# Kernel tuning notes

Hardware: AMD Instinct MI355X
Metric: run time of the kernel (lower is better)

The kernel has to match this reference:

```python
import jax, jax.numpy as jnp
import numpy as np
from jax import lax

DIM = 1024
DIM_INNER = 2048  # int(dim * expansion_factor)


def log_g(x):
    # log-space g(x): where(x>=0, log(relu(x)+0.5), -softplus(-x))
    return jnp.where(x >= 0, jnp.log(jax.nn.relu(x) + 0.5), -jax.nn.softplus(-x))


def heinsen_associative_scan_log(log_coeffs, log_values):
    # parallel log-space linear recurrence over the sequence axis (axis=1)
    a_star = jnp.cumsum(log_coeffs, axis=1)
    log_h0_plus_b_star = lax.cumlogsumexp(log_values - a_star, axis=1)
    return a_star + log_h0_plus_b_star


def setup_inputs() -> dict:
    key = jax.random.key(0)
    k_x, k_w1, k_w2 = jax.random.split(key, 3)
    x = jax.random.normal(k_x, (4, 4096, DIM), dtype=jnp.float32)
    # Linear(dim, 2*dim_inner, bias=False): store as [in, out] for x @ W
    W_hg = jax.random.normal(k_w1, (DIM, 2 * DIM_INNER), dtype=jnp.float32) * (1.0 / np.sqrt(DIM))
    W_out = jax.random.normal(k_w2, (DIM_INNER, DIM), dtype=jnp.float32) * (1.0 / np.sqrt(DIM_INNER))
    return {"x": x, "W_hg": W_hg, "W_out": W_out}


def reference(x, W_hg, W_out):
    # x: [b, s, dim]
    hg = jnp.einsum('bsd,de->bse', x, W_hg)  # [b, s, 2*dim_inner]
    hidden, gate = jnp.split(hg, 2, axis=-1)
    log_coeffs = -jax.nn.softplus(gate)        # log(1 - z)
    log_z = -jax.nn.softplus(-gate)            # log z
    log_values = log_z + log_g(hidden)
    log_h = heinsen_associative_scan_log(log_coeffs, log_values)  # [b, s, dim_inner]
    out = jnp.exp(log_h)
    return jnp.einsum('bse,ed->bsd', out, W_out)
```

## Files before the change

### kernel.cpp

```cpp
#include <hip/hip_runtime.h>
#include <cmath>

#define DIM 1024
#define DIM_INNER 2048
#define BATCH 4
#define SEQ 4096
#define MTOT (BATCH * SEQ)
#define CHUNK 32
#define NCHUNK (SEQ / CHUNK)

typedef __bf16 bf16x8 __attribute__((ext_vector_type(8)));
typedef short short8_t __attribute__((ext_vector_type(8)));
typedef float floatx4 __attribute__((ext_vector_type(4)));
typedef unsigned short u16x4 __attribute__((ext_vector_type(4)));
typedef unsigned int uint4_t __attribute__((ext_vector_type(4)));
typedef float float4_t __attribute__((ext_vector_type(4)));
typedef unsigned short ushort_t;

template <int N> struct IC { static constexpr int v = N; };
template <bool B> struct BC { static constexpr bool v = B; };

#define LGKM_SB(n) do { asm volatile("s_waitcnt lgkmcnt(" #n ")" ::: "memory"); \
                        __builtin_amdgcn_sched_barrier(0); } while (0)
#define SCHED0() __builtin_amdgcn_sched_barrier(0)
#define SBAR() __builtin_amdgcn_s_barrier()
#define PRIO1() __builtin_amdgcn_s_setprio(1)
#define PRIO0() __builtin_amdgcn_s_setprio(0)

__device__ __forceinline__ unsigned short f2bf(float f) {
  unsigned int u = __builtin_bit_cast(unsigned int, f);
  u += 0x7fffu + ((u >> 16) & 1u);
  return (unsigned short)(u >> 16);
}
__device__ __forceinline__ float bflo2f(unsigned int u) {
  return __builtin_bit_cast(float, u << 16);
}
__device__ __forceinline__ float bfhi2f(unsigned int u) {
  return __builtin_bit_cast(float, u & 0xffff0000u);
}

__device__ __forceinline__ void lclv_fast(float h, float g, float& lc, float& lv) {
  float eg = __expf(-fabsf(g));
  float sp = fmaxf(g, 0.f) + __logf(1.f + eg);
  lc = -sp;
  float eh = __expf(h);
  float t  = (h >= 0.f) ? (h + 0.5f) : (1.f + eh);
  float lt = __logf(t);
  float lg = (h >= 0.f) ? lt : (h - lt);
  lv = g + lc + lg;
}
__device__ __forceinline__ float logaddexp_f(float a, float b) {
  float m = fmaxf(a, b);
  return m + __logf(1.f + __expf(-fabsf(a - b)));
}

__device__ __forceinline__ void async_copy16(const ushort_t* g, ushort_t* l) {
  __builtin_amdgcn_global_load_lds(
      (const __attribute__((address_space(1))) void*)g,
      (__attribute__((address_space(3))) void*)l, 16, 0, 0);
}

__global__ __launch_bounds__(256) void convert_f32_bf16(
    const float* __restrict__ src, ushort_t* __restrict__ dst) {
  int i = blockIdx.x * 256 + threadIdx.x;
  float4 v = ((const float4*)src)[i];
  u16x4 o = {f2bf(v.x), f2bf(v.y), f2bf(v.z), f2bf(v.w)};
  ((u16x4*)dst)[i] = o;
}

__global__ __launch_bounds__(256) void transpose_f32_bf16(
    const float* __restrict__ src, ushort_t* __restrict__ dst, int K, int N) {
  __shared__ float tile[32][33];
  int tx = threadIdx.x & 31, ty = threadIdx.x >> 5;
  int n0 = blockIdx.x * 32, k0 = blockIdx.y * 32;
#pragma unroll
  for (int i = 0; i < 4; i++) {
    int k = ty + i * 8;
    tile[k][tx] = src[(size_t)(k0 + k) * N + n0 + tx];
  }
  __syncthreads();
#pragma unroll
  for (int i = 0; i < 4; i++) {
    int r = ty + i * 8;
    dst[(size_t)(n0 + r) * K + k0 + tx] = f2bf(tile[tx][r]);
  }
}

#define G1_NT (DIM / 64)
#define G2_NT (DIM_INNER / 64)

__global__ __launch_bounds__(512, 2) void gemm1_fused(
    const ushort_t* __restrict__ Xbf, const ushort_t* __restrict__ Wt,
    unsigned int* __restrict__ LCLV,
    float* __restrict__ Asum, float* __restrict__ Lend, int nbch) {
  __shared__ __align__(16) ushort_t lds[81920];

  const int tid = threadIdx.x;
  const int wv = tid >> 6;
  const int lane = tid & 63;
  const int wr = wv >> 2;
  const int wc = wv & 3;
  const int l15 = lane & 15;
  const int quad = lane >> 4;
  const int n0 = blockIdx.x * 128;
  const int m0 = blockIdx.y * 256;

  int aSrc[2][2], bSrc[2][2];
  int dstE[2];
#pragma unroll
  for (int L = 0; L < 2; L++) {
    int e = L * 512 + tid;
    int row = e >> 3, slot = e & 7;
    int sw = (slot ^ (row & 7)) << 3;
    dstE[L] = e * 8;
#pragma unroll
    for (int half = 0; half < 2; half++) {
      aSrc[half][L] = (m0 + half * 128 + row) * DIM + sw;
      int br = half * 128 + row;
      int grow = n0 + ((br >> 6) << 5) + (br & 31) + ((br & 32) ? DIM_INNER : 0);
      bSrc[half][L] = grow * DIM + sw;
    }
  }

  auto stageA = [&](int kt, int half, int buf) {
#pragma unroll
    for (int L = 0; L < 2; L++)
      async_copy16(Xbf + aSrc[half][L] + kt * 64,
                   lds + buf * 16384 + half * 8192 + dstE[L]);
  };
  auto stageB = [&](int kt, int half, int buf) {
#pragma unroll
    for (int L = 0; L < 2; L++)
      async_copy16(Wt + bSrc[half][L] + kt * 64,
                   lds + 49152 + buf * 16384 + half * 8192 + dstE[L]);
  };

  const int swz0 = ((quad ^ (l15 & 7)) << 3);
  const int swz1 = (((4 | quad) ^ (l15 & 7)) << 3);
  const int aB0 = wr * 8192 + l15 * 64 + swz0;
  const int aB1 = wr * 8192 + l15 * 64 + swz1;
  const int bB0 = wc * 4096 + l15 * 64 + swz0;
  const int bB1 = wc * 4096 + l15 * 64 + swz1;

  auto readA = [&](int buf, int mf, int ks) -> bf16x8 {
    const ushort_t* p = lds + buf * 16384 + (ks ? aB1 : aB0) + mf * 1024;
    return __builtin_bit_cast(bf16x8, *(const short8_t*)p);
  };
  auto readB = [&](int buf, int nf, int ks) -> bf16x8 {
    const ushort_t* p = lds + 49152 + buf * 16384 + (ks ? bB1 : bB0) + nf * 1024;
    return __builtin_bit_cast(bf16x8, *(const short8_t*)p);
  };

  floatx4 acc[8][4];
#pragma unroll
  for (int i = 0; i < 8; i++)
#pragma unroll
    for (int j = 0; j < 4; j++) acc[i][j] = (floatx4){0.f, 0.f, 0.f, 0.f};

  bf16x8 aF[4][2], b0F[2][2], b1F[2][2];

  auto mma4 = [&](auto MA, auto MC, auto J, bf16x8 (&bX)[2][2]) {
#pragma unroll
    for (int jj = 0; jj < 2; jj++)
#pragma unroll
      for (int ks = 0; ks < 2; ks++)
        acc[MC.v][J.v + jj] = __builtin_amdgcn_mfma_f32_16x16x32_bf16(
            aF[MA.v][ks], bX[jj][ks], acc[MC.v][J.v + jj], 0, 0, 0);
  };
  auto mmaRow = [&](auto J, bf16x8 (&bvec)[2]) {
#pragma unroll
    for (int m = 0; m < 4; m++)
#pragma unroll
      for (int ks = 0; ks < 2; ks++)
        acc[m][J.v] = __builtin_amdgcn_mfma_f32_16x16x32_bf16(
            aF[m][ks], bvec[ks], acc[m][J.v], 0, 0, 0);
  };

  int bufA = 0, bufB = 0, bufAn = 2, bufBn = 1;

  auto tileBody = [&](int kb, int ka, auto STB, auto STA, auto VMALL) {
    aF[0][0] = readA(bufA, 0, 0); aF[0][1] = readA(bufA, 0, 1);
    b0F[0][0] = readB(bufB, 0, 0); b0F[0][1] = readB(bufB, 0, 1);
    b0F[1][0] = readB(bufB, 1, 0); b0F[1][1] = readB(bufB, 1, 1);
    SCHED0();
    aF[1][0] = readA(bufA, 1, 0); aF[1][1] = readA(bufA, 1, 1);
    SCHED0();
    aF[2][0] = readA(bufA, 2, 0); aF[2][1] = readA(bufA, 2, 1);
    SCHED0();
    aF[3][0] = readA(bufA, 3, 0); aF[3][1] = readA(bufA, 3, 1);
    SCHED0();
    if constexpr (STB.v) stageB(kb, 0, bufBn);
    SBAR();
    PRIO1();
    LGKM_SB(6); mma4(IC<0>{}, IC<0>{}, IC<0>{}, b0F);
    LGKM_SB(4); mma4(IC<1>{}, IC<1>{}, IC<0>{}, b0F);
    LGKM_SB(2); mma4(IC<2>{}, IC<2>{}, IC<0>{}, b0F);
    LGKM_SB(0); mma4(IC<3>{}, IC<3>{}, IC<0>{}, b0F);
    PRIO0();
    SBAR();

    b1F[0][0] = readB(bufB, 2, 0); b1F[0][1] = readB(bufB, 2, 1);
    SCHED0();
    b1F[1][0] = readB(bufB, 3, 0); b1F[1][1] = readB(bufB, 3, 1);
    SCHED0();
    if constexpr (STB.v) stageB(kb, 1, bufBn);
    SBAR();
    PRIO1();
    LGKM_SB(2); mmaRow(IC<2>{}, b1F[0]);
    LGKM_SB(0); mmaRow(IC<3>{}, b1F[1]);
    PRIO0();
    SBAR();

    aF[0][0] = readA(bufA, 4, 0); aF[0][1] = readA(bufA, 4, 1);
    SCHED0();
    aF[1][0] = readA(bufA, 5, 0); aF[1][1] = readA(bufA, 5, 1);
    SCHED0();
    aF[2][0] = readA(bufA, 6, 0); aF[2][1] = readA(bufA, 6, 1);
    SCHED0();
    aF[3][0] = readA(bufA, 7, 0); aF[3][1] = readA(bufA, 7, 1);
    SCHED0();
    if constexpr (STA.v) stageA(ka, 0, bufAn);
    SBAR();
    PRIO1();
    LGKM_SB(6); mma4(IC<0>{}, IC<4>{}, IC<2>{}, b1F);
    LGKM_SB(4); mma4(IC<1>{}, IC<5>{}, IC<2>{}, b1F);
    LGKM_SB(2); mma4(IC<2>{}, IC<6>{}, IC<2>{}, b1F);
    LGKM_SB(0); mma4(IC<3>{}, IC<7>{}, IC<2>{}, b1F);
    PRIO0();
    SBAR();

    if constexpr (STA.v) stageA(ka, 1, bufAn);
    SCHED0();
    if constexpr (STA.v) {
      asm volatile("s_waitcnt vmcnt(4)" ::: "memory");
    } else if constexpr (VMALL.v) {
      asm volatile("s_waitcnt vmcnt(0)" ::: "memory");
    }
    SBAR();
    PRIO1();
    mma4(IC<0>{}, IC<4>{}, IC<0>{}, b0F);
    mma4(IC<1>{}, IC<5>{}, IC<0>{}, b0F);
    mma4(IC<2>{}, IC<6>{}, IC<0>{}, b0F);
    mma4(IC<3>{}, IC<7>{}, IC<0>{}, b0F);
    PRIO0();
    SBAR();
  };

  stageB(0, 0, 0); stageB(0, 1, 0);
  stageA(0, 0, 0); stageA(0, 1, 0);
  stageA(1, 0, 1); stageA(1, 1, 1);
  asm volatile("s_waitcnt vmcnt(4)" ::: "memory");
  SBAR();

  for (int u = 0; u < G1_NT - 2; u++) {
    tileBody(u + 1, u + 2, BC<true>{}, BC<true>{}, BC<false>{});
    bufA = (bufA == 2) ? 0 : bufA + 1;
    bufAn = (bufAn == 2) ? 0 : bufAn + 1;
    bufB ^= 1; bufBn ^= 1;
  }
  tileBody(G1_NT - 1, 0, BC<true>{}, BC<false>{}, BC<true>{});
  bufA = (bufA == 2) ? 0 : bufA + 1;
  bufB ^= 1;
  tileBody(0, 0, BC<false>{}, BC<false>{}, BC<false>{});

#pragma unroll
  for (int c2 = 0; c2 < 4; c2++) {
    float hA[2][2], hL[2][2];
#pragma unroll
    for (int mh = 0; mh < 2; mh++) {
      int mf = c2 * 2 + mh;
#pragma unroll
      for (int j = 0; j < 2; j++) {
        int col = n0 + wc * 32 + j * 16 + l15;
        float sA = 0.f, sL = -INFINITY;
#pragma unroll
        for (int r = 0; r < 4; r++) {
          int row = m0 + wr * 128 + mf * 16 + quad * 4 + r;
          float lc, lv;
          lclv_fast(acc[mf][j][r], acc[mf][j + 2][r], lc, lv);
          unsigned int pk = ((unsigned int)f2bf(lv) << 16) | (unsigned int)f2bf(lc);
          LCLV[(size_t)row * DIM_INNER + col] = pk;
          sL = logaddexp_f(sL + lc, lv);
          sA += lc;
        }
        float A = sA, L = sL;
#pragma unroll
        for (int st = 16; st <= 32; st <<= 1) {
          float Ao = __shfl_xor(A, st, 64);
          float Lo = __shfl_xor(L, st, 64);
          bool upper = (lane & st) != 0;
          L = upper ? logaddexp_f(Lo + A, L) : logaddexp_f(L + Ao, Lo);
          A = A + Ao;
        }
        hA[mh][j] = A;
        hL[mh][j] = L;
      }
    }
#pragma unroll
    for (int j = 0; j < 2; j++) {
      float A = hA[0][j] + hA[1][j];
      float L = logaddexp_f(hL[0][j] + hA[1][j], hL[1][j]);
      if (quad == 0) {
        int cg = (m0 + wr * 128 + c2 * 32) >> 5;
        int bz = cg >> 7;
        int cs = cg & (NCHUNK - 1);
        int col = n0 + wc * 32 + j * 16 + l15;
        size_t sidx = (size_t)cs * nbch + (size_t)bz * DIM_INNER + col;
        Asum[sidx] = A;
        Lend[sidx] = L;
      }
    }
  }
}

#define A0OFF 0
#define A1OFF 16384
#define B0OFF 32768
#define B1OFF 49152

__global__ __launch_bounds__(512, 2) void gemm2(
    const ushort_t* __restrict__ Hbf, const ushort_t* __restrict__ Wot,
    float* __restrict__ OUT) {
  __shared__ __align__(16) ushort_t lds[65536];

  const int tid = threadIdx.x;
  const int lane = tid & 63;
  const int wv = tid >> 6;
  const int wr = wv >> 2;
  const int wc = wv & 3;
  const int l15 = lane & 15;
  const int quad = lane >> 4;
  const int n0 = blockIdx.x * 256;
  const int m0 = blockIdx.y * 256;

  int aSrc[2][2], bSrc[2][2];
  int dstE[2];
#pragma unroll
  for (int L = 0; L < 2; L++) {
    int e = L * 512 + tid;
    int row = e >> 3, slot = e & 7;
    int sw = (slot ^ (row & 7)) << 3;
    dstE[L] = e * 8;
#pragma unroll
    for (int half = 0; half < 2; half++) {
      aSrc[half][L] = (m0 + half * 128 + row) * DIM_INNER + sw;
      bSrc[half][L] = (n0 + half * 128 + row) * DIM_INNER + sw;
    }
  }

  auto stA = [&](int kt, int half, auto AO) {
#pragma unroll
    for (int L = 0; L < 2; L++)
      async_copy16(Hbf + aSrc[half][L] + kt * 64,
                   lds + AO.v + half * 8192 + dstE[L]);
  };
  auto stB = [&](int kt, int half, auto BO) {
#pragma unroll
    for (int L = 0; L < 2; L++)
      async_copy16(Wot + bSrc[half][L] + kt * 64,
                   lds + BO.v + half * 8192 + dstE[L]);
  };

  const int swz0 = ((quad ^ (l15 & 7)) << 3);
  const int swz1 = (((4 | quad) ^ (l15 & 7)) << 3);
  const int aB0 = wr * 8192 + l15 * 64 + swz0;
  const int aB1 = wr * 8192 + l15 * 64 + swz1;
  const int bB0 = wc * 4096 + l15 * 64 + swz0;
  const int bB1 = wc * 4096 + l15 * 64 + swz1;

  floatx4 acc[8][4];
#pragma unroll
  for (int i = 0; i < 8; i++)
#pragma unroll
    for (int j = 0; j < 4; j++) acc[i][j] = (floatx4){0.f, 0.f, 0.f, 0.f};

  bf16x8 aF[4][2], b0F[2][2], b1F[2][2];

  auto rdA4 = [&](auto AO, int mb) {
#pragma unroll
    for (int m = 0; m < 4; m++) {
      aF[m][0] = __builtin_bit_cast(bf16x8,
          *(const short8_t*)(lds + AO.v + aB0 + (mb + m) * 1024));
      aF[m][1] = __builtin_bit_cast(bf16x8,
          *(const short8_t*)(lds + AO.v + aB1 + (mb + m) * 1024));
    }
  };
  auto rdB2 = [&](auto BO, int nb, bf16x8 (&bX)[2][2]) {
#pragma unroll
    for (int n = 0; n < 2; n++) {
      bX[n][0] = __builtin_bit_cast(bf16x8,
          *(const short8_t*)(lds + BO.v + bB0 + (nb + n) * 1024));
      bX[n][1] = __builtin_bit_cast(bf16x8,
          *(const short8_t*)(lds + BO.v + bB1 + (nb + n) * 1024));
    }
  };
  auto mmaQ = [&](auto MB, auto JB, bf16x8 (&bX)[2][2]) {
#pragma unroll
    for (int m = 0; m < 4; m++)
#pragma unroll
      for (int jj = 0; jj < 2; jj++)
#pragma unroll
        for (int ks = 0; ks < 2; ks++)
          acc[MB.v + m][JB.v + jj] = __builtin_amdgcn_mfma_f32_16x16x32_bf16(
              aF[m][ks], bX[jj][ks], acc[MB.v + m][JB.v + jj], 0, 0, 0);
  };

  auto pairBody = [&](int k2, auto STG) {
    rdA4(IC<A0OFF>{}, 0); rdB2(IC<B0OFF>{}, 0, b0F);
    SCHED0();
    SBAR(); LGKM_SB(0);
    PRIO1(); mmaQ(IC<0>{}, IC<0>{}, b0F); PRIO0();
    SBAR();
    rdB2(IC<B0OFF>{}, 2, b1F);
    SCHED0();
    SBAR(); LGKM_SB(0);
    PRIO1(); mmaQ(IC<0>{}, IC<2>{}, b1F); PRIO0();
    SBAR();
    rdA4(IC<A0OFF>{}, 4);
    SCHED0();
    if constexpr (STG.v) stB(k2, 0, IC<B0OFF>{});
    SBAR(); LGKM_SB(0);
    PRIO1(); mmaQ(IC<4>{}, IC<2>{}, b1F); PRIO0();
    SBAR();
    if constexpr (STG.v) {
      stB(k2, 1, IC<B0OFF>{});
      asm volatile("s_waitcnt vmcnt(4)" ::: "memory");
    } else {
      asm volatile("s_waitcnt vmcnt(0)" ::: "memory");
    }
    SBAR();
    PRIO1(); mmaQ(IC<4>{}, IC<0>{}, b0F); PRIO0();
    SBAR();
    rdA4(IC<A1OFF>{}, 0); rdB2(IC<B1OFF>{}, 0, b0F);
    SCHED0();
    if constexpr (STG.v) stA(k2, 0, IC<A0OFF>{});
    SBAR(); LGKM_SB(0);
    PRIO1(); mmaQ(IC<0>{}, IC<0>{}, b0F); PRIO0();
    SBAR();
    rdB2(IC<B1OFF>{}, 2, b1F);
    SCHED0();
    if constexpr (STG.v) stA(k2, 1, IC<A0OFF>{});
    SBAR(); LGKM_SB(0);
    PRIO1(); mmaQ(IC<0>{}, IC<2>{}, b1F); PRIO0();
    SBAR();
    rdA4(IC<A1OFF>{}, 4);
    SCHED0();
    if constexpr (STG.v) stB(k2 + 1, 0, IC<B1OFF>{});
    SBAR(); LGKM_SB(0);
    PRIO1(); mmaQ(IC<4>{}, IC<2>{}, b1F); PRIO0();
    SBAR();
    if constexpr (STG.v) {
      stB(k2 + 1, 1, IC<B1OFF>{});
      stA(k2 + 1, 0, IC<A1OFF>{});
      stA(k2 + 1, 1, IC<A1OFF>{});
      asm volatile("s_waitcnt vmcnt(8)" ::: "memory");
    }
    SBAR();
    PRIO1(); mmaQ(IC<4>{}, IC<0>{}, b0F); PRIO0();
    SBAR();
  };

  stA(0, 0, IC<A0OFF>{}); stA(0, 1, IC<A0OFF>{});
  stB(0, 0, IC<B0OFF>{}); stB(0, 1, IC<B0OFF>{});
  stA(1, 0, IC<A1OFF>{}); stA(1, 1, IC<A1OFF>{});
  stB(1, 0, IC<B1OFF>{}); stB(1, 1, IC<B1OFF>{});
  asm volatile("s_waitcnt vmcnt(8)" ::: "memory");
  SBAR();

  for (int it = 0; it < G2_NT / 2 - 1; ++it)
    pairBody(2 * it + 2, BC<true>{});
  pairBody(0, BC<false>{});

#pragma unroll
  for (int mf = 0; mf < 8; mf++)
#pragma unroll
    for (int j = 0; j < 4; j++) {
      int col = n0 + wc * 64 + (j >> 1) * 32 + (j & 1) * 16 + l15;
#pragma unroll
      for (int r = 0; r < 4; r++) {
        int row = m0 + wr * 128 + mf * 16 + quad * 4 + r;
        OUT[(size_t)row * DIM + col] = acc[mf][j][r];
      }
    }
}


__global__ __launch_bounds__(256) void scan_phase2(
    float* Asum, const float* __restrict__ Lend, int nbch) {
  int ch = blockIdx.x * 256 + threadIdx.x;
  float p = -INFINITY;
  for (int c = 0; c < NCHUNK; c++) {
    float a = Asum[(size_t)c * nbch + ch];
    float le = Lend[(size_t)c * nbch + ch];
    Asum[(size_t)c * nbch + ch] = p;
    p = logaddexp_f(a + p, le);
  }
}

__global__ __launch_bounds__(256) void scan_phase3(
    const unsigned int* __restrict__ LCLV, const float* __restrict__ P,
    ushort_t* __restrict__ H, int nbch) {
  const int EQ = DIM_INNER / 4;
  int tid = blockIdx.x * 256 + threadIdx.x;
  int ep = tid % EQ;
  int tmp = tid / EQ;
  int c = tmp % NCHUNK;
  int bz = tmp / NCHUNK;
  size_t base4 = ((size_t)bz * SEQ + (size_t)c * CHUNK) * EQ + ep;
  const uint4_t* L4 = (const uint4_t*)LCLV;
  u16x4* H4 = (u16x4*)H;

  size_t pidx = ((size_t)c * nbch + (size_t)bz * DIM_INNER) / 4 + ep;
  float4_t logh = ((const float4_t*)P)[pidx];
#pragma unroll 4
  for (int t = 0; t < CHUNK; t++) {
    uint4_t u = L4[base4 + (size_t)t * EQ];
    u16x4 hv;
#pragma unroll
    for (int k = 0; k < 4; k++) {
      float lc = bflo2f(u[k]), lv = bfhi2f(u[k]);
      logh[k] = logaddexp_f(lc + logh[k], lv);
      hv[k] = f2bf(__expf(logh[k]));
    }
    H4[base4 + (size_t)t * EQ] = hv;
  }
}

extern "C" void kernel_launch(void* const* d_in, const int* in_sizes, int n_in,
                              void* d_out, int out_size, void* d_ws, size_t ws_size,
                              hipStream_t stream) {
  const float* X = (const float*)d_in[0];
  const float* Whg = (const float*)d_in[1];
  const float* Wout = (const float*)d_in[2];
  float* out = (float*)d_out;

  ushort_t* Xbf = (ushort_t*)d_ws;
  ushort_t* Whg_t = Xbf + (size_t)MTOT * DIM;
  ushort_t* Wout_t = Whg_t + (size_t)(2 * DIM_INNER) * DIM;
  char* pp = (char*)(Wout_t + (size_t)DIM * DIM_INNER);

  const size_t fixed_bytes = (size_t)MTOT * DIM * 2 +
                             (size_t)2 * DIM_INNER * DIM * 2 +
                             (size_t)DIM * DIM_INNER * 2;
  const size_t per_batch = (size_t)SEQ * DIM_INNER * 4 +
                           (size_t)SEQ * DIM_INNER * 2 +
                           2 * (size_t)DIM_INNER * NCHUNK * 4;
  int nb = 4;
  while (nb > 1 && fixed_bytes + (size_t)nb * per_batch > ws_size) nb >>= 1;
  const int npass = BATCH / nb;

  convert_f32_bf16<<<(MTOT * DIM / 4) / 256, 256, 0, stream>>>(X, Xbf);
  transpose_f32_bf16<<<dim3(2 * DIM_INNER / 32, DIM / 32), 256, 0, stream>>>(
      Whg, Whg_t, DIM, 2 * DIM_INNER);
  transpose_f32_bf16<<<dim3(DIM / 32, DIM_INNER / 32), 256, 0, stream>>>(
      Wout, Wout_t, DIM_INNER, DIM);

  for (int pass = 0; pass < npass; pass++) {
    const int b0 = pass * nb;
    const int nrows = nb * SEQ;
    const int nbch = nb * DIM_INNER;

    unsigned int* LCLV = (unsigned int*)pp;
    ushort_t* Hbf = (ushort_t*)(LCLV + (size_t)nb * SEQ * DIM_INNER);
    float* Asum = (float*)(Hbf + (size_t)nb * SEQ * DIM_INNER);
    float* Lend = Asum + (size_t)nb * DIM_INNER * NCHUNK;

    gemm1_fused<<<dim3(DIM_INNER / 128, nrows / 256), 512, 0, stream>>>(
        Xbf + (size_t)b0 * SEQ * DIM, Whg_t, LCLV, Asum, Lend, nbch);
    scan_phase2<<<nbch / 256, 256, 0, stream>>>(Asum, Lend, nbch);
    scan_phase3<<<(nbch / 4 * NCHUNK) / 256, 256, 0, stream>>>(LCLV, Asum, Hbf, nbch);
    gemm2<<<dim3(DIM / 256, nrows / 256), 512, 0, stream>>>(
        Hbf, Wout_t, out + (size_t)b0 * SEQ * DIM);
  }
}
```

Before: 447.2 us.

## Unfuse chunk summary scan from GEMM1 epilogue into separate phase1 kernel

Moves the per-chunk scan summary (sum of log coefficients and log-sum-exp end value) out of the GEMM1 epilogue into a new scan_phase1 kernel that re-reads the packed LCLV buffer. This makes the GEMM epilogue lighter, dropping its cross-lane shuffles and transcendental work, which may also ease register pressure. In exchange it costs an extra launch and a full extra read of LCLV. Phase2 is also changed to batch eight chunk loads before its serial recurrence, to hide memory latency.

```diff
diff --git a/kernel.cpp b/kernel.cpp
--- a/kernel.cpp
+++ b/kernel.cpp
@@ -91,8 +91,7 @@
 
 __global__ __launch_bounds__(512, 2) void gemm1_fused(
     const ushort_t* __restrict__ Xbf, const ushort_t* __restrict__ Wt,
-    unsigned int* __restrict__ LCLV,
-    float* __restrict__ Asum, float* __restrict__ Lend, int nbch) {
+    unsigned int* __restrict__ LCLV) {
   __shared__ __align__(16) ushort_t lds[81920];
 
   const int tid = threadIdx.x;
@@ -264,53 +263,19 @@
   tileBody(0, 0, BC<false>{}, BC<false>{}, BC<false>{});
 
 #pragma unroll
-  for (int c2 = 0; c2 < 4; c2++) {
-    float hA[2][2], hL[2][2];
-#pragma unroll
-    for (int mh = 0; mh < 2; mh++) {
-      int mf = c2 * 2 + mh;
-#pragma unroll
-      for (int j = 0; j < 2; j++) {
-        int col = n0 + wc * 32 + j * 16 + l15;
-        float sA = 0.f, sL = -INFINITY;
-#pragma unroll
-        for (int r = 0; r < 4; r++) {
-          int row = m0 + wr * 128 + mf * 16 + quad * 4 + r;
-          float lc, lv;
-          lclv_fast(acc[mf][j][r], acc[mf][j + 2][r], lc, lv);
-          unsigned int pk = ((unsigned int)f2bf(lv) << 16) | (unsigned int)f2bf(lc);
-          LCLV[(size_t)row * DIM_INNER + col] = pk;
-          sL = logaddexp_f(sL + lc, lv);
-          sA += lc;
-        }
-        float A = sA, L = sL;
-#pragma unroll
-        for (int st = 16; st <= 32; st <<= 1) {
-          float Ao = __shfl_xor(A, st, 64);
-          float Lo = __shfl_xor(L, st, 64);
-          bool upper = (lane & st) != 0;
-          L = upper ? logaddexp_f(Lo + A, L) : logaddexp_f(L + Ao, Lo);
-          A = A + Ao;
-        }
-        hA[mh][j] = A;
-        hL[mh][j] = L;
+  for (int mf = 0; mf < 8; mf++)
+#pragma unroll
+    for (int j = 0; j < 2; j++) {
+      int col = n0 + wc * 32 + j * 16 + l15;
+#pragma unroll
+      for (int r = 0; r < 4; r++) {
+        int row = m0 + wr * 128 + mf * 16 + quad * 4 + r;
+        float lc, lv;
+        lclv_fast(acc[mf][j][r], acc[mf][j + 2][r], lc, lv);
+        unsigned int pk = ((unsigned int)f2bf(lv) << 16) | (unsigned int)f2bf(lc);
+        LCLV[(size_t)row * DIM_INNER + col] = pk;
       }
     }
-#pragma unroll
-    for (int j = 0; j < 2; j++) {
-      float A = hA[0][j] + hA[1][j];
-      float L = logaddexp_f(hL[0][j] + hA[1][j], hL[1][j]);
-      if (quad == 0) {
-        int cg = (m0 + wr * 128 + c2 * 32) >> 5;
-        int bz = cg >> 7;
-        int cs = cg & (NCHUNK - 1);
-        int col = n0 + wc * 32 + j * 16 + l15;
-        size_t sidx = (size_t)cs * nbch + (size_t)bz * DIM_INNER + col;
-        Asum[sidx] = A;
-        Lend[sidx] = L;
-      }
-    }
-  }
 }
 
 #define A0OFF 0
@@ -484,16 +449,51 @@
     }
 }
 
+__global__ __launch_bounds__(256) void scan_phase1(
+    const unsigned int* __restrict__ LCLV,
+    float* __restrict__ Asum, float* __restrict__ Lend, int nbch) {
+  const int EQ = DIM_INNER / 4;
+  int tid = blockIdx.x * 256 + threadIdx.x;
+  int ep = tid % EQ;
+  int tmp = tid / EQ;
+  int c = tmp % NCHUNK;
+  int bz = tmp / NCHUNK;
+  size_t base4 = ((size_t)bz * SEQ + (size_t)c * CHUNK) * EQ + ep;
+  const uint4_t* L4 = (const uint4_t*)LCLV;
+
+  float4_t asum = {0.f, 0.f, 0.f, 0.f};
+  float4_t logh = {-INFINITY, -INFINITY, -INFINITY, -INFINITY};
+#pragma unroll 4
+  for (int t = 0; t < CHUNK; t++) {
+    uint4_t u = L4[base4 + (size_t)t * EQ];
+#pragma unroll
+    for (int k = 0; k < 4; k++) {
+      float lc = bflo2f(u[k]), lv = bfhi2f(u[k]);
+      asum[k] += lc;
+      logh[k] = logaddexp_f(lc + logh[k], lv);
+    }
+  }
+  size_t sidx = ((size_t)c * nbch + (size_t)bz * DIM_INNER) / 4 + ep;
+  ((float4_t*)Asum)[sidx] = asum;
+  ((float4_t*)Lend)[sidx] = logh;
+}
 
 __global__ __launch_bounds__(256) void scan_phase2(
     float* Asum, const float* __restrict__ Lend, int nbch) {
   int ch = blockIdx.x * 256 + threadIdx.x;
   float p = -INFINITY;
-  for (int c = 0; c < NCHUNK; c++) {
-    float a = Asum[(size_t)c * nbch + ch];
-    float le = Lend[(size_t)c * nbch + ch];
-    Asum[(size_t)c * nbch + ch] = p;
-    p = logaddexp_f(a + p, le);
+  for (int c8 = 0; c8 < NCHUNK; c8 += 8) {
+    float a[8], le[8];
+#pragma unroll
+    for (int i = 0; i < 8; i++) {
+      a[i]  = Asum[(size_t)(c8 + i) * nbch + ch];
+      le[i] = Lend[(size_t)(c8 + i) * nbch + ch];
+    }
+#pragma unroll
+    for (int i = 0; i < 8; i++) {
+      Asum[(size_t)(c8 + i) * nbch + ch] = p;
+      p = logaddexp_f(a[i] + p, le[i]);
+    }
   }
 }
 
@@ -566,7 +566,8 @@
     float* Lend = Asum + (size_t)nb * DIM_INNER * NCHUNK;
 
     gemm1_fused<<<dim3(DIM_INNER / 128, nrows / 256), 512, 0, stream>>>(
-        Xbf + (size_t)b0 * SEQ * DIM, Whg_t, LCLV, Asum, Lend, nbch);
+        Xbf + (size_t)b0 * SEQ * DIM, Whg_t, LCLV);
+    scan_phase1<<<(nbch / 4 * NCHUNK) / 256, 256, 0, stream>>>(LCLV, Asum, Lend, nbch);
     scan_phase2<<<nbch / 256, 256, 0, stream>>>(Asum, Lend, nbch);
     scan_phase3<<<(nbch / 4 * NCHUNK) / 256, 256, 0, stream>>>(LCLV, Asum, Hbf, nbch);
     gemm2<<<dim3(DIM / 256, nrows / 256), 512, 0, stream>>>(
```

New measurement: 421.4 us. 5.8% less time.
